# Performance work log

Hardware: AMD Instinct MI355X
Metric: run time of the kernel (lower is better)

Reference implementation:

```python
import jax, jax.numpy as jnp
import numpy as np

N_NODES = 50000
N_EDGES = 800000
IN_FEATS = 256
NUM_HEADS = 4
OUT_FEATS = 64
ALPHA = 0.2  # leaky-relu negative slope


def setup_inputs() -> dict:
    key = jax.random.key(0)
    k1, k2, k3, k4, k5, k6 = jax.random.split(key, 6)
    feat = jax.random.normal(k1, (N_NODES, IN_FEATS), dtype=jnp.float32)
    # fc weight stored as [in, heads*out] (transpose of torch Linear layout)
    fc_w = jax.random.normal(k2, (IN_FEATS, NUM_HEADS * OUT_FEATS), dtype=jnp.float32) * 0.05
    attn_l = jax.random.normal(k3, (1, NUM_HEADS, OUT_FEATS), dtype=jnp.float32) * 0.1
    attn_r = jax.random.normal(k4, (1, NUM_HEADS, OUT_FEATS), dtype=jnp.float32) * 0.1
    src = jax.random.randint(k5, (N_EDGES,), 0, N_NODES, dtype=jnp.int32)
    dst = jax.random.randint(k6, (N_EDGES,), 0, N_NODES, dtype=jnp.int32)
    return {"feat": feat, "fc_w": fc_w, "attn_l": attn_l, "attn_r": attn_r,
            "src": src, "dst": dst}


def reference(feat, fc_w, attn_l, attn_r, src, dst):
    # Linear projection -> [N, H, D]
    ft = (feat @ fc_w).reshape(-1, NUM_HEADS, OUT_FEATS)
    # Per-node attention logits (split GAT attention vector): [N, H]
    el = (ft * attn_l).sum(-1)
    er = (ft * attn_r).sum(-1)
    # Edge scores: u_add_v + leaky_relu -> [E, H]
    e = jax.nn.leaky_relu(el[src] + er[dst], negative_slope=ALPHA)
    # edge_softmax: softmax over incoming edges of each destination node
    e_max = jax.ops.segment_max(e, dst, num_segments=N_NODES)  # [N, H]
    e_exp = jnp.exp(e - e_max[dst])                            # [E, H]
    e_sum = jax.ops.segment_sum(e_exp, dst, num_segments=N_NODES)  # [N, H]
    a = e_exp / e_sum[dst]                                     # [E, H]
    # u_mul_e + sum aggregation: [E, H, D] messages scatter-added to dst
    msg = ft[src] * a[:, :, None]
    rst = jax.ops.segment_sum(msg, dst, num_segments=N_NODES)  # [N, H, D]
    return rst
```

## Files before the change

kernel.cpp:

```cpp
#include <hip/hip_runtime.h>
#include <hip/hip_bf16.h>
#include <hip/hip_fp16.h>

#define N_NODES 50000
#define N_EDGES 800000
#define IN_F 256
#define NH 4
#define DH 64
#define HD 256
#define ALPHA 0.2f
#define EPB 16384
#define NHB ((N_EDGES + EPB - 1) / EPB)
#define GEMMB ((N_NODES + 255) / 256)

typedef short bf16x8 __attribute__((ext_vector_type(8)));
typedef float f32x4 __attribute__((ext_vector_type(4)));

__device__ __forceinline__ unsigned short f2bf(float f) {
    unsigned u = __float_as_uint(f);
    u = (u + 0x7FFFu + ((u >> 16) & 1u)) >> 16;
    return (unsigned short)u;
}

__global__ __launch_bounds__(256) void k_cvt(const float* __restrict__ fw,
                                             unsigned short* __restrict__ Bt) {
    int n = blockIdx.x;
    int k = threadIdx.x;
    Bt[n * 256 + k] = f2bf(fw[k * 256 + n]);
}

__global__ __launch_bounds__(512) void k_main(const float* __restrict__ A,
                                              const unsigned short* __restrict__ Bt,
                                              unsigned short* __restrict__ fth,
                                              float* __restrict__ el,
                                              float* __restrict__ er,
                                              const float* __restrict__ al,
                                              const float* __restrict__ ar,
                                              const int* __restrict__ dst,
                                              int* __restrict__ hist,
                                              int* __restrict__ erank, int M) {
    __shared__ __align__(16) char smem[131072];
    const int tid = threadIdx.x;

    if (blockIdx.x < NHB) {
        int* cnt = (int*)smem;
        const int b = blockIdx.x;
        for (int i = tid; i < N_NODES / 2; i += 512) cnt[i] = 0;
        __syncthreads();
        const int e0 = b * EPB;
        const int eend = min(e0 + EPB, N_EDGES);
        for (int e = e0 + tid; e < eend; e += 512) {
            int d = dst[e];
            int old = atomicAdd(&cnt[d >> 1], (d & 1) ? (1 << 16) : 1);
            erank[e] = (d & 1) ? ((old >> 16) & 0xffff) : (old & 0xffff);
        }
        __syncthreads();
        int* hb = hist + (size_t)b * N_NODES;
        for (int i = tid; i < N_NODES / 2; i += 512) {
            int v = cnt[i];
            int2 o; o.x = v & 0xffff; o.y = ((unsigned)v) >> 16;
            *(int2*)(hb + 2 * i) = o;
        }
        return;
    }

    const int m0 = (blockIdx.x - NHB) * 256;

    #pragma unroll
    for (int c = 0; c < 16; c++) {
        int o = c * 8192 + tid * 16;
        bf16x8 v = *(const bf16x8*)((const char*)Bt + o);
        int nl = o >> 9;
        int lb = o ^ ((nl & 7) << 4);
        *(bf16x8*)(smem + lb) = v;
    }
    __syncthreads();

    const int w = tid >> 6, lane = tid & 63;
    const int wm = w >> 2, wn = w & 3;
    const int fr = lane & 15, quad = lane >> 4;

    const float* arow[8];
    int gm[8];
    #pragma unroll
    for (int j = 0; j < 8; j++) {
        gm[j] = m0 + wm * 128 + j * 16 + fr;
        int cr = gm[j] < M ? gm[j] : (M - 1);
        arow[j] = A + (size_t)cr * IN_F;
    }

    f32x4 acc[8][4];
    #pragma unroll
    for (int j = 0; j < 8; j++)
        #pragma unroll
        for (int f = 0; f < 4; f++) acc[j][f] = (f32x4){0.f, 0.f, 0.f, 0.f};

    #pragma unroll
    for (int kk = 0; kk < 8; kk++) {
        bf16x8 af[8];
        #pragma unroll
        for (int j = 0; j < 8; j++) {
            float4 lo = *(const float4*)(arow[j] + kk * 32 + quad * 8);
            float4 hi = *(const float4*)(arow[j] + kk * 32 + quad * 8 + 4);
            af[j][0] = (short)f2bf(lo.x); af[j][1] = (short)f2bf(lo.y);
            af[j][2] = (short)f2bf(lo.z); af[j][3] = (short)f2bf(lo.w);
            af[j][4] = (short)f2bf(hi.x); af[j][5] = (short)f2bf(hi.y);
            af[j][6] = (short)f2bf(hi.z); af[j][7] = (short)f2bf(hi.w);
        }
        #pragma unroll
        for (int f = 0; f < 4; f++) {
            int nl = wn * 64 + f * 16 + fr;
            int lb = (nl * 512 + (kk * 32 + quad * 8) * 2) ^ ((nl & 7) << 4);
            bf16x8 bfr = *(const bf16x8*)(smem + lb);
            #pragma unroll
            for (int j = 0; j < 8; j++)
                acc[j][f] = __builtin_amdgcn_mfma_f32_16x16x32_bf16(bfr, af[j], acc[j][f], 0, 0, 0);
        }
    }

    #pragma unroll
    for (int j = 0; j < 8; j++) {
        float pl = 0.f, pr = 0.f;
        #pragma unroll
        for (int f = 0; f < 4; f++) {
            float4 a4 = *(const float4*)(al + wn * 64 + f * 16 + quad * 4);
            float4 b4 = *(const float4*)(ar + wn * 64 + f * 16 + quad * 4);
            pl += acc[j][f][0] * a4.x + acc[j][f][1] * a4.y + acc[j][f][2] * a4.z + acc[j][f][3] * a4.w;
            pr += acc[j][f][0] * b4.x + acc[j][f][1] * b4.y + acc[j][f][2] * b4.z + acc[j][f][3] * b4.w;
        }
        pl += __shfl_xor(pl, 16); pl += __shfl_xor(pl, 32);
        pr += __shfl_xor(pr, 16); pr += __shfl_xor(pr, 32);
        if (quad == 0 && gm[j] < M) {
            el[gm[j] * NH + wn] = pl;
            er[gm[j] * NH + wn] = pr;
        }
    }

    #pragma unroll
    for (int j = 0; j < 8; j++) {
        if (gm[j] < M) {
            unsigned short* dp = fth + (size_t)gm[j] * HD + wn * 64 + quad * 4;
            #pragma unroll
            for (int f = 0; f < 4; f++) {
                ushort4 pk;
                pk.x = __half_as_ushort(__float2half(acc[j][f][0]));
                pk.y = __half_as_ushort(__float2half(acc[j][f][1]));
                pk.z = __half_as_ushort(__float2half(acc[j][f][2]));
                pk.w = __half_as_ushort(__float2half(acc[j][f][3]));
                *(ushort4*)(dp + f * 16) = pk;
            }
        }
    }
}

__global__ __launch_bounds__(512) void k_scan1(int* __restrict__ hist,
                                               int* __restrict__ counts,
                                               int* __restrict__ incl,
                                               int* __restrict__ bsum, int N) {
    __shared__ int sm[512];
    int i = blockIdx.x * 512 + threadIdx.x;
    int v = 0;
    if (i < N) {
        int pf = 0;
        for (int c = 0; c < NHB; c++) {
            int t = hist[(size_t)c * N_NODES + i];
            hist[(size_t)c * N_NODES + i] = pf;
            pf += t;
        }
        v = pf;
        counts[i] = v;
    }
    sm[threadIdx.x] = v;
    __syncthreads();
    for (int off = 1; off < 512; off <<= 1) {
        int t = (threadIdx.x >= off) ? sm[threadIdx.x - off] : 0;
        __syncthreads();
        sm[threadIdx.x] += t;
        __syncthreads();
    }
    if (i < N) incl[i] = sm[threadIdx.x];
    if (threadIdx.x == 511) bsum[blockIdx.x] = sm[511];
}

__global__ __launch_bounds__(256) void k_scan3(const int* __restrict__ counts,
                                               const int* __restrict__ incl,
                                               const int* __restrict__ bsum,
                                               int* __restrict__ offs, int N) {
    __shared__ int sprefix;
    int nb = blockIdx.x >> 1;
    if (threadIdx.x < 64) {
        int v = 0;
        for (int j = threadIdx.x; j < nb; j += 64) v += bsum[j];
        #pragma unroll
        for (int off = 1; off < 64; off <<= 1) v += __shfl_xor(v, off);
        if (threadIdx.x == 0) sprefix = v;
    }
    __syncthreads();
    int i = blockIdx.x * 256 + threadIdx.x;
    if (i < N) offs[i] = incl[i] - counts[i] + sprefix;
}

__global__ __launch_bounds__(256) void k_scatter(const int* __restrict__ src,
                                                 const int* __restrict__ dst,
                                                 const int* __restrict__ hist,
                                                 const int* __restrict__ offs,
                                                 const int* __restrict__ erank,
                                                 int* __restrict__ esrc) {
    int e = blockIdx.x * 256 + threadIdx.x;
    if (e < N_EDGES) {
        int d = dst[e];
        int c = e >> 14;
        int p = hist[(size_t)c * N_NODES + d] + offs[d] + erank[e];
        esrc[p] = src[e];
    }
}

__global__ __launch_bounds__(256) void k_agg(const unsigned short* __restrict__ fth,
                                             const float* __restrict__ el,
                                             const float* __restrict__ er,
                                             const int* __restrict__ offs,
                                             const int* __restrict__ counts,
                                             const int* __restrict__ esrc,
                                             float* __restrict__ out, int N) {
    int wid = (blockIdx.x * 256 + threadIdx.x) >> 6;
    const int lane = threadIdx.x & 63;
    if (wid >= N) return;
    const int deg = counts[wid];
    const int start = offs[wid];
    const int quad = lane >> 4;
    const float erq = er[wid * NH + quad];

    float s = 0.f;
    float a0 = 0.f, a1 = 0.f, a2 = 0.f, a3 = 0.f;
    #pragma unroll 4
    for (int i = 0; i < deg; i++) {
        int sv = esrc[start + i];
        float x = el[sv * NH + quad] + erq;
        x = (x > 0.f) ? x : ALPHA * x;
        float wgt = __expf(x);
        s += wgt;
        float2 raw = ((const float2*)fth)[(size_t)sv * 64 + lane];
        __half2 h0 = *reinterpret_cast<const __half2*>(&raw.x);
        __half2 h1 = *reinterpret_cast<const __half2*>(&raw.y);
        a0 = fmaf(wgt, __low2float(h0), a0);
        a1 = fmaf(wgt, __high2float(h0), a1);
        a2 = fmaf(wgt, __low2float(h1), a2);
        a3 = fmaf(wgt, __high2float(h1), a3);
    }
    float invd = (deg > 0 && s > 0.f) ? 1.f / s : 0.f;
    f32x4 o;
    o[0] = a0 * invd; o[1] = a1 * invd; o[2] = a2 * invd; o[3] = a3 * invd;
    __builtin_nontemporal_store(o, (f32x4*)out + (size_t)wid * 64 + lane);
}

extern "C" void kernel_launch(void* const* d_in, const int* in_sizes, int n_in,
                              void* d_out, int out_size, void* d_ws, size_t ws_size,
                              hipStream_t stream) {
    const float* feat = (const float*)d_in[0];
    const float* fc_w = (const float*)d_in[1];
    const float* attn_l = (const float*)d_in[2];
    const float* attn_r = (const float*)d_in[3];
    const int* src = (const int*)d_in[4];
    const int* dst = (const int*)d_in[5];
    float* out = (float*)d_out;

    char* w = (char*)d_ws;
    unsigned short* fth = (unsigned short*)w;  w += (size_t)N_NODES * HD * 2;
    unsigned short* Bt = (unsigned short*)w;   w += (size_t)IN_F * HD * 2;
    float* el = (float*)w;       w += (size_t)N_NODES * NH * 4;
    float* er = (float*)w;       w += (size_t)N_NODES * NH * 4;
    int* hist = (int*)w;         w += (size_t)NHB * N_NODES * 4;
    int* counts = (int*)w;       w += (size_t)N_NODES * 4;
    int* incl = (int*)w;         w += (size_t)N_NODES * 4;
    int* offs = (int*)w;         w += (size_t)N_NODES * 4;
    int* bsum = (int*)w;         w += 1024;
    int* erank = (int*)w;        w += (size_t)N_EDGES * 4;
    int* esrc = (int*)w;         w += (size_t)N_EDGES * 4;

    k_cvt<<<256, 256, 0, stream>>>(fc_w, Bt);

    k_main<<<NHB + GEMMB, 512, 0, stream>>>(feat, Bt, fth, el, er, attn_l, attn_r,
                                            dst, hist, erank, N_NODES);

    int nsb = (N_NODES + 511) / 512;
    k_scan1<<<nsb, 512, 0, stream>>>(hist, counts, incl, bsum, N_NODES);
    k_scan3<<<(N_NODES + 255) / 256, 256, 0, stream>>>(counts, incl, bsum, offs, N_NODES);

    int eblocks = (N_EDGES + 255) / 256;
    k_scatter<<<eblocks, 256, 0, stream>>>(src, dst, hist, offs, erank, esrc);

    int agg_blocks = (N_NODES * 64 + 255) / 256;
    k_agg<<<agg_blocks, 256, 0, stream>>>(fth, el, er, offs, counts, esrc, out, N_NODES);
}
```

Before: 145.7 us.

## Shrink CSR build buffers to 16-bit and merge scan kernels via atomic cursor

Stores per-block histograms and per-edge ranks as 16-bit values instead of 32-bit, roughly halving the memory traffic of the CSR construction. The two-pass prefix scan becomes a single kernel. Each block claims its base offset from a global atomic cursor, which k_cvt resets, so the incl and bsum buffers and one launch go away. The scatter kernel now handles four edges per thread with vector loads. Node ranges are no longer laid out in node order, which is fine because aggregation reads offs and counts per node, but the layout is nondeterministic and relies on counts fitting in 16 bits.

Result: no change. 142.9 us (-2.0%).

```diff
diff --git a/kernel.cpp b/kernel.cpp
--- a/kernel.cpp
+++ b/kernel.cpp
@@ -23,7 +23,9 @@
 }
 
 __global__ __launch_bounds__(256) void k_cvt(const float* __restrict__ fw,
-                                             unsigned short* __restrict__ Bt) {
+                                             unsigned short* __restrict__ Bt,
+                                             int* __restrict__ gcursor) {
+    if (blockIdx.x == 0 && threadIdx.x == 0) *gcursor = 0;
     int n = blockIdx.x;
     int k = threadIdx.x;
     Bt[n * 256 + k] = f2bf(fw[k * 256 + n]);
@@ -37,8 +39,8 @@
                                               const float* __restrict__ al,
                                               const float* __restrict__ ar,
                                               const int* __restrict__ dst,
-                                              int* __restrict__ hist,
-                                              int* __restrict__ erank, int M) {
+                                              unsigned short* __restrict__ hist16,
+                                              unsigned short* __restrict__ erank16, int M) {
     __shared__ __align__(16) char smem[131072];
     const int tid = threadIdx.x;
 
@@ -52,15 +54,12 @@
         for (int e = e0 + tid; e < eend; e += 512) {
             int d = dst[e];
             int old = atomicAdd(&cnt[d >> 1], (d & 1) ? (1 << 16) : 1);
-            erank[e] = (d & 1) ? ((old >> 16) & 0xffff) : (old & 0xffff);
-        }
-        __syncthreads();
-        int* hb = hist + (size_t)b * N_NODES;
-        for (int i = tid; i < N_NODES / 2; i += 512) {
-            int v = cnt[i];
-            int2 o; o.x = v & 0xffff; o.y = ((unsigned)v) >> 16;
-            *(int2*)(hb + 2 * i) = o;
-        }
+            erank16[e] = (unsigned short)((d & 1) ? ((old >> 16) & 0xffff) : (old & 0xffff));
+        }
+        __syncthreads();
+        int4* hb = (int4*)(hist16 + (size_t)b * N_NODES);
+        for (int i = tid; i < N_NODES / 8; i += 512)
+            hb[i] = ((const int4*)cnt)[i];
         return;
     }
 
@@ -153,18 +152,20 @@
     }
 }
 
-__global__ __launch_bounds__(512) void k_scan1(int* __restrict__ hist,
-                                               int* __restrict__ counts,
-                                               int* __restrict__ incl,
-                                               int* __restrict__ bsum, int N) {
+__global__ __launch_bounds__(512) void k_scan(unsigned short* __restrict__ hist16,
+                                              int* __restrict__ counts,
+                                              int* __restrict__ offs,
+                                              int* __restrict__ gcursor, int N) {
     __shared__ int sm[512];
+    __shared__ int sbase;
     int i = blockIdx.x * 512 + threadIdx.x;
     int v = 0;
     if (i < N) {
         int pf = 0;
         for (int c = 0; c < NHB; c++) {
-            int t = hist[(size_t)c * N_NODES + i];
-            hist[(size_t)c * N_NODES + i] = pf;
+            unsigned short* p = hist16 + (size_t)c * N_NODES + i;
+            int t = *p;
+            *p = (unsigned short)pf;
             pf += t;
         }
         v = pf;
@@ -178,41 +179,28 @@
         sm[threadIdx.x] += t;
         __syncthreads();
     }
-    if (i < N) incl[i] = sm[threadIdx.x];
-    if (threadIdx.x == 511) bsum[blockIdx.x] = sm[511];
-}
-
-__global__ __launch_bounds__(256) void k_scan3(const int* __restrict__ counts,
-                                               const int* __restrict__ incl,
-                                               const int* __restrict__ bsum,
-                                               int* __restrict__ offs, int N) {
-    __shared__ int sprefix;
-    int nb = blockIdx.x >> 1;
-    if (threadIdx.x < 64) {
-        int v = 0;
-        for (int j = threadIdx.x; j < nb; j += 64) v += bsum[j];
-        #pragma unroll
-        for (int off = 1; off < 64; off <<= 1) v += __shfl_xor(v, off);
-        if (threadIdx.x == 0) sprefix = v;
-    }
+    if (threadIdx.x == 511) sbase = atomicAdd(gcursor, sm[511]);
     __syncthreads();
-    int i = blockIdx.x * 256 + threadIdx.x;
-    if (i < N) offs[i] = incl[i] - counts[i] + sprefix;
+    if (i < N) offs[i] = sbase + sm[threadIdx.x] - v;
 }
 
 __global__ __launch_bounds__(256) void k_scatter(const int* __restrict__ src,
                                                  const int* __restrict__ dst,
-                                                 const int* __restrict__ hist,
+                                                 const unsigned short* __restrict__ hist16,
                                                  const int* __restrict__ offs,
-                                                 const int* __restrict__ erank,
+                                                 const unsigned short* __restrict__ erank16,
                                                  int* __restrict__ esrc) {
-    int e = blockIdx.x * 256 + threadIdx.x;
-    if (e < N_EDGES) {
-        int d = dst[e];
-        int c = e >> 14;
-        int p = hist[(size_t)c * N_NODES + d] + offs[d] + erank[e];
-        esrc[p] = src[e];
-    }
+    int t = blockIdx.x * 256 + threadIdx.x;
+    if (t >= N_EDGES / 4) return;
+    int e = t * 4;
+    const unsigned short* hp = hist16 + (size_t)(e >> 14) * N_NODES;
+    int4 d4 = *(const int4*)(dst + e);
+    int4 s4 = *(const int4*)(src + e);
+    ushort4 r4 = *(const ushort4*)(erank16 + e);
+    esrc[hp[d4.x] + offs[d4.x] + r4.x] = s4.x;
+    esrc[hp[d4.y] + offs[d4.y] + r4.y] = s4.y;
+    esrc[hp[d4.z] + offs[d4.z] + r4.z] = s4.z;
+    esrc[hp[d4.w] + offs[d4.w] + r4.w] = s4.w;
 }
 
 __global__ __launch_bounds__(256) void k_agg(const unsigned short* __restrict__ fth,
@@ -269,25 +257,23 @@
     unsigned short* Bt = (unsigned short*)w;   w += (size_t)IN_F * HD * 2;
     float* el = (float*)w;       w += (size_t)N_NODES * NH * 4;
     float* er = (float*)w;       w += (size_t)N_NODES * NH * 4;
-    int* hist = (int*)w;         w += (size_t)NHB * N_NODES * 4;
+    unsigned short* hist16 = (unsigned short*)w;  w += (size_t)NHB * N_NODES * 2;
     int* counts = (int*)w;       w += (size_t)N_NODES * 4;
-    int* incl = (int*)w;         w += (size_t)N_NODES * 4;
     int* offs = (int*)w;         w += (size_t)N_NODES * 4;
-    int* bsum = (int*)w;         w += 1024;
-    int* erank = (int*)w;        w += (size_t)N_EDGES * 4;
+    int* gcursor = (int*)w;      w += 256;
+    unsigned short* erank16 = (unsigned short*)w; w += (size_t)N_EDGES * 2;
     int* esrc = (int*)w;         w += (size_t)N_EDGES * 4;
 
-    k_cvt<<<256, 256, 0, stream>>>(fc_w, Bt);
+    k_cvt<<<256, 256, 0, stream>>>(fc_w, Bt, gcursor);
 
     k_main<<<NHB + GEMMB, 512, 0, stream>>>(feat, Bt, fth, el, er, attn_l, attn_r,
-                                            dst, hist, erank, N_NODES);
-
-    int nsb = (N_NODES + 511) / 512;
-    k_scan1<<<nsb, 512, 0, stream>>>(hist, counts, incl, bsum, N_NODES);
-    k_scan3<<<(N_NODES + 255) / 256, 256, 0, stream>>>(counts, incl, bsum, offs, N_NODES);
-
-    int eblocks = (N_EDGES + 255) / 256;
-    k_scatter<<<eblocks, 256, 0, stream>>>(src, dst, hist, offs, erank, esrc);
+                                            dst, hist16, erank16, N_NODES);
+
+    k_scan<<<(N_NODES + 511) / 512, 512, 0, stream>>>(hist16, counts, offs,
+                                                      gcursor, N_NODES);
+
+    k_scatter<<<(N_EDGES / 4 + 255) / 256, 256, 0, stream>>>(src, dst, hist16,
+                                                             offs, erank16, esrc);
 
     int agg_blocks = (N_NODES * 64 + 255) / 256;
     k_agg<<<agg_blocks, 256, 0, stream>>>(fth, el, er, offs, counts, esrc, out, N_NODES);
```
